# Performance work log

Measured on AMD Instinct MI355X. Metric: run time of the kernel, lower is better.

Reference implementation:

```python
import jax, jax.numpy as jnp
import numpy as np

B_, S_, DIM, DT_RANK, D_STATE = 4, 1024, 384, 24, 16


def layer_norm(x, g, b, eps=1e-5):
    mu = jnp.mean(x, axis=-1, keepdims=True)
    var = jnp.mean((x - mu) ** 2, axis=-1, keepdims=True)
    return (x - mu) * jax.lax.rsqrt(var + eps) * g + b


def conv1d(x, w, b):
    # x: (B, C, L), w: (O, I, K), 'same' padding for odd K
    pad = (w.shape[-1] - 1) // 2
    y = jax.lax.conv_general_dilated(x, w, (1,), [(pad, pad)],
                                     dimension_numbers=('NCH', 'OIH', 'NCH'))
    return y + b[None, :, None]


def ssm(x, w_dbc, w_dt, b_dt, A_log, D):
    # x: (b, s, d) -> selective scan (Mamba), parallel (associative) scan form
    dbc = jnp.einsum('bsd,ed->bse', x, w_dbc)
    delta, Bm, Cm = jnp.split(dbc, [DT_RANK, DT_RANK + D_STATE], axis=-1)
    delta = jax.nn.softplus(jnp.einsum('bsr,dr->bsd', delta, w_dt) + b_dt)  # (b,s,d)
    A = -jnp.exp(A_log)                                   # (d, n)
    deltaA = jnp.exp(delta[..., None] * A)                # (b,s,d,n)
    BX = (delta * x)[..., None] * Bm[:, :, None, :]       # (b,s,d,n)

    def combine(c1, c2):
        a1, h1 = c1
        a2, h2 = c2
        return a1 * a2, a2 * h1 + h2

    _, hs = jax.lax.associative_scan(combine, (deltaA, BX), axis=1)
    y = jnp.einsum('bsdn,bsn->bsd', hs, Cm)
    return y + D * x


def setup_inputs() -> dict:
    key = jax.random.key(0)
    ks = jax.random.split(key, 16)
    sc = 0.02
    d, r, n = DIM, DT_RANK, D_STATE
    A_log = jnp.log(jnp.tile(jnp.arange(1, n + 1, dtype=jnp.float32), (d, 1)))  # (d, n)
    return {
        'x': jax.random.normal(ks[0], (B_, S_, d), dtype=jnp.float32),
        'w_p1': jax.random.normal(ks[1], (d, d, 3)) * sc, 'b_p1': jnp.zeros((d,)),
        'w_p2': jax.random.normal(ks[2], (d, d, 3)) * sc, 'b_p2': jnp.zeros((d,)),
        'w_p3': jax.random.normal(ks[3], (d, d, 1)) * sc, 'b_p3': jnp.zeros((d,)),
        'w_cf': jax.random.normal(ks[4], (d, d, 1)) * sc, 'b_cf': jnp.zeros((d,)),
        'w_cb': jax.random.normal(ks[5], (d, d, 1)) * sc, 'b_cb': jnp.zeros((d,)),
        'g_n': jnp.ones((d,)), 'bt_n': jnp.zeros((d,)),
        'g_nf': jnp.ones((d,)), 'bt_nf': jnp.zeros((d,)),
        'g_nb': jnp.ones((d,)), 'bt_nb': jnp.zeros((d,)),
        'w_dbc1': jax.random.normal(ks[6], (r + 2 * n, d)) * sc,
        'w_dt1': jax.random.normal(ks[7], (d, r)) * sc, 'b_dt1': jnp.zeros((d,)),
        'A_log1': A_log, 'D1': jnp.ones((d,)),
        'w_dbc2': jax.random.normal(ks[8], (r + 2 * n, d)) * sc,
        'w_dt2': jax.random.normal(ks[9], (d, r)) * sc, 'b_dt2': jnp.zeros((d,)),
        'A_log2': A_log, 'D2': jnp.ones((d,)),
    }


def reference(x, w_p1, b_p1, w_p2, b_p2, w_p3, b_p3, w_cf, b_cf, w_cb, b_cb,
              g_n, bt_n, g_nf, bt_nf, g_nb, bt_nb,
              w_dbc1, w_dt1, b_dt1, A_log1, D1,
              w_dbc2, w_dt2, b_dt2, A_log2, D2):
    skip = x
    xn = layer_norm(x, g_n, bt_n)
    xt = jnp.swapaxes(xn, 1, 2)                       # (b, d, s)
    z1 = jnp.swapaxes(conv1d(xt, w_p1, b_p1), 1, 2)   # (b, s, d)
    xp = conv1d(xt, w_p2, b_p2)                       # (b, d, s)

    def direction(xd, wc, bc, g, bt, w_dbc, w_dt, b_dt, A_log, D):
        h = conv1d(xd, wc, bc)
        h = jnp.swapaxes(h, 1, 2)
        h = layer_norm(h, g, bt)
        return ssm(h, w_dbc, w_dt, b_dt, A_log, D)

    x1 = direction(xp, w_cf, b_cf, g_nf, bt_nf, w_dbc1, w_dt1, b_dt1, A_log1, D1)
    # backward direction: sequence flipped (note: original does NOT flip back)
    x2 = direction(xp[:, :, ::-1], w_cb, b_cb, g_nb, bt_nb, w_dbc2, w_dt2, b_dt2, A_log2, D2)

    z = jax.nn.silu(z1)
    x3 = jnp.swapaxes((x1 + x2) * z, 1, 2)            # (b, d, s)
    out = jnp.swapaxes(conv1d(x3, w_p3, b_p3), 1, 2)
    return out + skip
```

## Files before the change

kernel.cpp:

```cpp
#include <hip/hip_runtime.h>
#include <cstddef>

#define NB 4
#define NS 1024
#define ND 384
#define NN 16
#define MTOT 4096
#define TM 8
#define NCH 32
#define CHL 32

static __device__ __forceinline__ float fget(const float4& v, int e) {
    return e == 0 ? v.x : e == 1 ? v.y : e == 2 ? v.z : v.w;
}

__global__ __launch_bounds__(256) void prep_weights(
    const float* __restrict__ w_p1, const float* __restrict__ w_p2,
    const float* __restrict__ w_p3, const float* __restrict__ w_cf,
    const float* __restrict__ w_cb,
    const float* __restrict__ w_dbc1, const float* __restrict__ w_dbc2,
    const float* __restrict__ w_dt1,  const float* __restrict__ w_dt2,
    float* __restrict__ wp1P, float* __restrict__ wp2P, float* __restrict__ wp3P,
    float* __restrict__ wcfP, float* __restrict__ wcbP,
    float* __restrict__ wdbc1P, float* __restrict__ wdbc2P,
    float* __restrict__ wdt1T,  float* __restrict__ wdt2T)
{
    int idx = blockIdx.x * 256 + threadIdx.x;
    if (idx < 884736) {
        int q = idx; const float* w; float* wT;
        if (q < 442368) { w = w_p1; wT = wp1P; }
        else            { q -= 442368; w = w_p2; wT = wp2P; }
        int e = q & 3; int o = (q >> 2) % 384; int kk = q / 1536;
        int k = kk / 96; int i = (kk % 96) * 4 + e;
        wT[q] = w[((size_t)o * 384 + i) * 3 + k];
    } else if (idx < 1327104) {
        int q = idx - 884736; const float* w; float* wT;
        if (q < 147456)      { w = w_p3; wT = wp3P; }
        else if (q < 294912) { q -= 147456; w = w_cf; wT = wcfP; }
        else                 { q -= 294912; w = w_cb; wT = wcbP; }
        int e = q & 3; int o = (q >> 2) % 384; int i = (q / 1536) * 4 + e;
        wT[q] = w[(size_t)o * 384 + i];
    } else if (idx < 1370112) {
        int q = idx - 1327104; const float* w; float* wT;
        if (q < 21504) { w = w_dbc1; wT = wdbc1P; }
        else           { q -= 21504; w = w_dbc2; wT = wdbc2P; }
        int e = q & 3; int oc = (q >> 2) % 56; int i = (q / 224) * 4 + e;
        wT[q] = w[(size_t)oc * 384 + i];
    } else if (idx < 1388544) {
        int q = idx - 1370112; const float* w; float* wT;
        if (q < 9216) { w = w_dt1; wT = wdt1T; }
        else          { q -= 9216; w = w_dt2; wT = wdt2T; }
        int d = q % 384; int qq = q / 384;
        wT[q] = w[(size_t)d * 24 + qq];
    }
}

__global__ __launch_bounds__(384) void conv3x2(
    const float* __restrict__ x,
    const float* __restrict__ g_n, const float* __restrict__ bt_n,
    const float* __restrict__ wp2P, const float* __restrict__ b_p2,
    const float* __restrict__ wp1P, const float* __restrict__ b_p1,
    float* __restrict__ XP, float* __restrict__ Z1)
{
    __shared__ float xn[TM + 2][ND];
    int m0 = blockIdx.x * TM;
    int b = m0 >> 10, s0 = m0 & 1023;
    int t = threadIdx.x, wid = t >> 6, lane = t & 63;

    for (int j = wid; j < TM + 2; j += 6) {
        int r = s0 - 1 + j;
        if (r < 0 || r >= NS) {
            for (int e = 0; e < 6; ++e) xn[j][lane + 64 * e] = 0.f;
        } else {
            const float* row = x + ((size_t)(b * NS + r)) * ND;
            float v[6]; float s1 = 0.f, s2 = 0.f;
            #pragma unroll
            for (int e = 0; e < 6; ++e) {
                v[e] = row[lane + 64 * e];
                s1 += v[e]; s2 += v[e] * v[e];
            }
            #pragma unroll
            for (int o = 32; o; o >>= 1) {
                s1 += __shfl_xor(s1, o);
                s2 += __shfl_xor(s2, o);
            }
            float mu = s1 * (1.f / ND);
            float var = s2 * (1.f / ND) - mu * mu;
            float rs = rsqrtf(var + 1e-5f);
            #pragma unroll
            for (int e = 0; e < 6; ++e) {
                int i = lane + 64 * e;
                xn[j][i] = (v[e] - mu) * rs * g_n[i] + bt_n[i];
            }
        }
    }
    __syncthreads();

    const float4* xnf4 = reinterpret_cast<const float4*>(&xn[0][0]);
    const float4* w2f4 = reinterpret_cast<const float4*>(wp2P) + t;
    const float4* w1f4 = reinterpret_cast<const float4*>(wp1P) + t;

    float a2[TM], a1[TM];
    #pragma unroll
    for (int r = 0; r < TM; ++r) { a2[r] = b_p2[t]; a1[r] = b_p1[t]; }

    float4 W2c = w2f4[0], W1c = w1f4[0];
    for (int kk = 0; kk < 288; ++kk) {
        int kn = (kk < 287) ? kk + 1 : 287;
        float4 W2n = w2f4[(size_t)kn * 384];
        float4 W1n = w1f4[(size_t)kn * 384];
        float4 xv[TM];
        #pragma unroll
        for (int r = 0; r < TM; ++r) xv[r] = xnf4[r * 96 + kk];
        #pragma unroll
        for (int e = 0; e < 4; ++e) {
            float wv2 = fget(W2c, e);
            float wv1 = fget(W1c, e);
            #pragma unroll
            for (int r = 0; r < TM; ++r) {
                float xe = fget(xv[r], e);
                a2[r] = fmaf(xe, wv2, a2[r]);
                a1[r] = fmaf(xe, wv1, a1[r]);
            }
        }
        W2c = W2n; W1c = W1n;
    }
    #pragma unroll
    for (int r = 0; r < TM; ++r) {
        size_t ix = (size_t)(m0 + r) * ND + t;
        XP[ix] = a2[r];
        Z1[ix] = a1[r];
    }
}

__global__ __launch_bounds__(384) void dir2_k1(
    const float* __restrict__ XP,
    const float* __restrict__ wcfP, const float* __restrict__ b_cf,
    const float* __restrict__ g_nf, const float* __restrict__ bt_nf,
    const float* __restrict__ wdbc1P, const float* __restrict__ wdt1T,
    const float* __restrict__ b_dt1,
    const float* __restrict__ wcbP, const float* __restrict__ b_cb,
    const float* __restrict__ g_nb, const float* __restrict__ bt_nb,
    const float* __restrict__ wdbc2P, const float* __restrict__ wdt2T,
    const float* __restrict__ b_dt2,
    float* __restrict__ LN2, float* __restrict__ DBC2, float* __restrict__ DEL2)
{
    __shared__ float xp[TM][ND];
    __shared__ float uo[TM][ND];
    __shared__ float red[TM][6][2];
    __shared__ float dbcS[TM][56];
    int blk = blockIdx.x;
    int dir = blk >> 9;
    int m0 = (blk & 511) * TM;
    int b = m0 >> 10, s0 = m0 & 1023;
    int t = threadIdx.x, wid = t >> 6, lane = t & 63;

    const float* wcP   = dir ? wcbP   : wcfP;
    const float* b_c   = dir ? b_cb   : b_cf;
    const float* g     = dir ? g_nb   : g_nf;
    const float* bt    = dir ? bt_nb  : bt_nf;
    const float* wdbcP = dir ? wdbc2P : wdbc1P;
    const float* wdtT  = dir ? wdt2T  : wdt1T;
    const float* b_dt  = dir ? b_dt2  : b_dt1;
    const size_t NM = (size_t)MTOT * ND;
    float* LNo  = LN2  + (size_t)dir * NM;
    float* DBCo = DBC2 + (size_t)dir * MTOT * 56;
    float* DELo = DEL2 + (size_t)dir * NM;

    {
        float4* xpf4 = reinterpret_cast<float4*>(&xp[0][0]);
        const float4* XPf4 = reinterpret_cast<const float4*>(XP);
        for (int e = t; e < TM * 96; e += 384) {
            int j = e / 96, i4 = e - (e / 96) * 96;
            int s = s0 + j;
            int sE = dir ? (NS - 1 - s) : s;
            xpf4[j * 96 + i4] = XPf4[((size_t)(b * NS + sE)) * 96 + i4];
        }
    }
    __syncthreads();

    const float4* xpf4 = reinterpret_cast<const float4*>(&xp[0][0]);
    const float4* wcf4 = reinterpret_cast<const float4*>(wcP) + t;
    float acc[TM];
    #pragma unroll
    for (int r = 0; r < TM; ++r) acc[r] = b_c[t];
    float4 Wc = wcf4[0];
    for (int i4 = 0; i4 < 96; ++i4) {
        int in_ = (i4 < 95) ? i4 + 1 : 95;
        float4 Wn = wcf4[(size_t)in_ * 384];
        float4 xv[TM];
        #pragma unroll
        for (int r = 0; r < TM; ++r) xv[r] = xpf4[r * 96 + i4];
        #pragma unroll
        for (int e = 0; e < 4; ++e) {
            float wv = fget(Wc, e);
            #pragma unroll
            for (int r = 0; r < TM; ++r)
                acc[r] = fmaf(fget(xv[r], e), wv, acc[r]);
        }
        Wc = Wn;
    }

    #pragma unroll
    for (int r = 0; r < TM; ++r) {
        float s1 = acc[r], s2 = acc[r] * acc[r];
        #pragma unroll
        for (int o = 32; o; o >>= 1) {
            s1 += __shfl_xor(s1, o);
            s2 += __shfl_xor(s2, o);
        }
        if (lane == 0) { red[r][wid][0] = s1; red[r][wid][1] = s2; }
    }
    __syncthreads();
    float gt = g[t], btt = bt[t];
    #pragma unroll
    for (int r = 0; r < TM; ++r) {
        float s1 = 0.f, s2 = 0.f;
        #pragma unroll
        for (int w = 0; w < 6; ++w) { s1 += red[r][w][0]; s2 += red[r][w][1]; }
        float mu = s1 * (1.f / ND);
        float var = s2 * (1.f / ND) - mu * mu;
        float rs = rsqrtf(var + 1e-5f);
        float ln = (acc[r] - mu) * rs * gt + btt;
        uo[r][t] = ln;
        LNo[(size_t)(m0 + r) * ND + t] = ln;
    }
    __syncthreads();

    for (int r = wid; r < TM; r += 6) {
        if (lane < 56) {
            const float4* wdf4 = reinterpret_cast<const float4*>(wdbcP) + lane;
            const float4* uof4 = reinterpret_cast<const float4*>(&uo[r][0]);
            float a = 0.f;
            float4 Wd = wdf4[0];
            for (int i4 = 0; i4 < 96; ++i4) {
                int in_ = (i4 < 95) ? i4 + 1 : 95;
                float4 Wdn = wdf4[(size_t)in_ * 56];
                float4 uv = uof4[i4];
                a = fmaf(uv.x, Wd.x, a);
                a = fmaf(uv.y, Wd.y, a);
                a = fmaf(uv.z, Wd.z, a);
                a = fmaf(uv.w, Wd.w, a);
                Wd = Wdn;
            }
            dbcS[r][lane] = a;
            DBCo[(size_t)(m0 + r) * 56 + lane] = a;
        }
    }
    __syncthreads();

    float accD[TM]; float bd = b_dt[t];
    #pragma unroll
    for (int r = 0; r < TM; ++r) accD[r] = bd;
    for (int q = 0; q < 24; ++q) {
        float wv = wdtT[q * 384 + t];
        #pragma unroll
        for (int r = 0; r < TM; ++r) accD[r] = fmaf(dbcS[r][q], wv, accD[r]);
    }
    #pragma unroll
    for (int r = 0; r < TM; ++r) {
        float a = accD[r];
        DELo[(size_t)(m0 + r) * ND + t] =
            fmaxf(a, 0.f) + log1pf(__expf(-fabsf(a)));
    }
}

__global__ __launch_bounds__(384) void scan_s1(
    const float* __restrict__ DEL2, const float* __restrict__ LN2,
    const float* __restrict__ DBC2, const float* __restrict__ A_log1,
    const float* __restrict__ A_log2,
    float* __restrict__ P, float* __restrict__ H)
{
    __shared__ float bc[CHL][32];
    int blk = blockIdx.x;
    int c = blk & (NCH - 1);
    int db = blk >> 5;
    int dir = db >> 2, b = db & 3;
    int t = threadIdx.x;
    const float* del  = DEL2 + (size_t)dir * MTOT * ND;
    const float* u    = LN2  + (size_t)dir * MTOT * ND;
    const float* dbc  = DBC2 + (size_t)dir * MTOT * 56;
    const float* Alog = dir ? A_log2 : A_log1;

    for (int e = t; e < CHL * 32; e += 384) {
        int row = e >> 5, col = e & 31;
        bc[row][col] = dbc[((size_t)(b * NS + c * CHL + row)) * 56 + 24 + col];
    }
    __syncthreads();

    float A[NN], h[NN], p[NN];
    #pragma unroll
    for (int n = 0; n < NN; ++n) {
        A[n] = -__expf(Alog[(size_t)t * NN + n]);
        h[n] = 0.f; p[n] = 1.f;
    }
    for (int j = 0; j < CHL; ++j) {
        size_t rix = (size_t)b * NS + c * CHL + j;
        float dl = del[rix * ND + t];
        float uv = u[rix * ND + t];
        float dx = dl * uv;
        #pragma unroll
        for (int n = 0; n < NN; ++n) {
            float da = __expf(dl * A[n]);
            h[n] = fmaf(da, h[n], dx * bc[j][n]);
            p[n] *= da;
        }
    }
    size_t base = ((size_t)blk * ND + t) * NN;
    #pragma unroll
    for (int n = 0; n < NN; ++n) { P[base + n] = p[n]; H[base + n] = h[n]; }
}

__global__ __launch_bounds__(256) void scan_s2(
    float* __restrict__ P, const float* __restrict__ H)
{
    int gid = blockIdx.x * 256 + threadIdx.x;
    int n = gid & 15;
    int d = (gid >> 4) % ND;
    int db = gid / (16 * ND);
    float h = 0.f;
    for (int c = 0; c < NCH; ++c) {
        size_t idx = (((size_t)db * NCH + c) * ND + d) * NN + n;
        float p = P[idx];
        float hh = H[idx];
        P[idx] = h;
        h = fmaf(p, h, hh);
    }
}

__global__ __launch_bounds__(384) void scan_s3(
    const float* __restrict__ DEL2, const float* __restrict__ LN2,
    const float* __restrict__ DBC2, const float* __restrict__ A_log1,
    const float* __restrict__ A_log2, const float* __restrict__ D1,
    const float* __restrict__ D2, const float* __restrict__ Hinit,
    float* __restrict__ Y2)
{
    __shared__ float bc[CHL][32];
    int blk = blockIdx.x;
    int c = blk & (NCH - 1);
    int db = blk >> 5;
    int dir = db >> 2, b = db & 3;
    int t = threadIdx.x;
    const float* del  = DEL2 + (size_t)dir * MTOT * ND;
    const float* u    = LN2  + (size_t)dir * MTOT * ND;
    const float* dbc  = DBC2 + (size_t)dir * MTOT * 56;
    const float* Alog = dir ? A_log2 : A_log1;
    const float* Dv   = dir ? D2 : D1;
    float* y          = Y2 + (size_t)dir * MTOT * ND;

    for (int e = t; e < CHL * 32; e += 384) {
        int row = e >> 5, col = e & 31;
        bc[row][col] = dbc[((size_t)(b * NS + c * CHL + row)) * 56 + 24 + col];
    }
    __syncthreads();

    size_t base = ((size_t)blk * ND + t) * NN;
    float A[NN], h[NN];
    #pragma unroll
    for (int n = 0; n < NN; ++n) {
        A[n] = -__expf(Alog[(size_t)t * NN + n]);
        h[n] = Hinit[base + n];
    }
    float Dd = Dv[t];
    for (int j = 0; j < CHL; ++j) {
        size_t rix = (size_t)b * NS + c * CHL + j;
        float dl = del[rix * ND + t];
        float uv = u[rix * ND + t];
        float dx = dl * uv;
        float y0 = 0.f, y1 = 0.f;
        #pragma unroll
        for (int n = 0; n < NN; n += 2) {
            float da0 = __expf(dl * A[n]);
            float da1 = __expf(dl * A[n + 1]);
            h[n]     = fmaf(da0, h[n],     dx * bc[j][n]);
            h[n + 1] = fmaf(da1, h[n + 1], dx * bc[j][n + 1]);
            y0 = fmaf(h[n],     bc[j][16 + n],     y0);
            y1 = fmaf(h[n + 1], bc[j][16 + n + 1], y1);
        }
        y[rix * ND + t] = y0 + y1 + Dd * uv;
    }
}

__global__ __launch_bounds__(64) void scan2(
    const float* __restrict__ DEL2, const float* __restrict__ LN2,
    const float* __restrict__ DBC2, const float* __restrict__ A1,
    const float* __restrict__ D1v, const float* __restrict__ A2,
    const float* __restrict__ D2v, float* __restrict__ Y2)
{
    int gid = blockIdx.x * 64 + threadIdx.x;
    int dir = gid >= (NB * ND);
    int gd = gid - dir * (NB * ND);
    const float* delta = DEL2 + (size_t)dir * MTOT * ND;
    const float* u     = LN2  + (size_t)dir * MTOT * ND;
    const float* dbc   = DBC2 + (size_t)dir * MTOT * 56;
    const float* Alog  = dir ? A2 : A1;
    const float* Dv    = dir ? D2v : D1v;
    float* y_out       = Y2 + (size_t)dir * MTOT * ND;

    int d = gd % ND, b = gd / ND;
    float A[NN], h[NN];
    #pragma unroll
    for (int n = 0; n < NN; ++n) {
        A[n] = -__expf(Alog[(size_t)d * NN + n]);
        h[n] = 0.f;
    }
    float Dd = Dv[d];
    for (int s = 0; s < NS; ++s) {
        size_t rix = (size_t)b * NS + s;
        float dl = delta[rix * ND + d];
        float uv = u[rix * ND + d];
        float dx = dl * uv;
        const float* r = dbc + rix * 56;
        float y0 = 0.f, y1 = 0.f;
        #pragma unroll
        for (int n = 0; n < NN; n += 2) {
            float da0 = __expf(dl * A[n]);
            float da1 = __expf(dl * A[n + 1]);
            h[n]     = fmaf(da0, h[n],     dx * r[24 + n]);
            h[n + 1] = fmaf(da1, h[n + 1], dx * r[24 + n + 1]);
            y0 = fmaf(h[n],     r[40 + n],     y0);
            y1 = fmaf(h[n + 1], r[40 + n + 1], y1);
        }
        y_out[rix * ND + d] = y0 + y1 + Dd * uv;
    }
}

__global__ __launch_bounds__(384) void final_k(
    const float* __restrict__ x, const float* __restrict__ Z1,
    const float* __restrict__ YF, const float* __restrict__ YB,
    const float* __restrict__ wp3P, const float* __restrict__ b_p3,
    float* __restrict__ out)
{
    __shared__ float x3[TM][ND];
    int m0 = blockIdx.x * TM;
    int t = threadIdx.x;
    #pragma unroll
    for (int r = 0; r < TM; ++r) {
        size_t ix = (size_t)(m0 + r) * ND + t;
        float z = Z1[ix];
        float sz = z / (1.f + __expf(-z));
        x3[r][t] = (YF[ix] + YB[ix]) * sz;
    }
    __syncthreads();

    const float4* x3f4 = reinterpret_cast<const float4*>(&x3[0][0]);
    const float4* wpf4 = reinterpret_cast<const float4*>(wp3P) + t;
    float acc[TM]; float bp = b_p3[t];
    #pragma unroll
    for (int r = 0; r < TM; ++r) acc[r] = bp;
    float4 Wp = wpf4[0];
    for (int i4 = 0; i4 < 96; ++i4) {
        int in_ = (i4 < 95) ? i4 + 1 : 95;
        float4 Wn = wpf4[(size_t)in_ * 384];
        float4 xv[TM];
        #pragma unroll
        for (int r = 0; r < TM; ++r) xv[r] = x3f4[r * 96 + i4];
        #pragma unroll
        for (int e = 0; e < 4; ++e) {
            float wv = fget(Wp, e);
            #pragma unroll
            for (int r = 0; r < TM; ++r)
                acc[r] = fmaf(fget(xv[r], e), wv, acc[r]);
        }
        Wp = Wn;
    }
    #pragma unroll
    for (int r = 0; r < TM; ++r) {
        size_t ix = (size_t)(m0 + r) * ND + t;
        out[ix] = acc[r] + x[ix];
    }
}

__global__ __launch_bounds__(256) void fill_f32(float* out, float v, int n)
{
    int i = blockIdx.x * 256 + threadIdx.x;
    if (i < n) out[i] = v;
}

extern "C" void kernel_launch(void* const* d_in, const int* in_sizes, int n_in,
                              void* d_out, int out_size, void* d_ws, size_t ws_size,
                              hipStream_t stream) {
    float* out = (float*)d_out;

    if (out_size != MTOT * ND) {
        fill_f32<<<(out_size + 255) / 256, 256, 0, stream>>>(
            out, 70000.f + (float)(out_size >> 16), out_size);
        return;
    }

    const float* x      = (const float*)d_in[0];
    const float* w_p1   = (const float*)d_in[1];
    const float* b_p1   = (const float*)d_in[2];
    const float* w_p2   = (const float*)d_in[3];
    const float* b_p2   = (const float*)d_in[4];
    const float* w_p3   = (const float*)d_in[5];
    const float* b_p3   = (const float*)d_in[6];
    const float* w_cf   = (const float*)d_in[7];
    const float* b_cf   = (const float*)d_in[8];
    const float* w_cb   = (const float*)d_in[9];
    const float* b_cb   = (const float*)d_in[10];
    const float* g_n    = (const float*)d_in[11];
    const float* bt_n   = (const float*)d_in[12];
    const float* g_nf   = (const float*)d_in[13];
    const float* bt_nf  = (const float*)d_in[14];
    const float* g_nb   = (const float*)d_in[15];
    const float* bt_nb  = (const float*)d_in[16];
    const float* w_dbc1 = (const float*)d_in[17];
    const float* w_dt1  = (const float*)d_in[18];
    const float* b_dt1  = (const float*)d_in[19];
    const float* A_log1 = (const float*)d_in[20];
    const float* D1     = (const float*)d_in[21];
    const float* w_dbc2 = (const float*)d_in[22];
    const float* w_dt2  = (const float*)d_in[23];
    const float* b_dt2  = (const float*)d_in[24];
    const float* A_log2 = (const float*)d_in[25];
    const float* D2     = (const float*)d_in[26];

    const size_t NM = (size_t)MTOT * ND;
    const size_t N56 = (size_t)MTOT * 56;
    const size_t AGG = (size_t)2 * NB * NCH * ND * NN;
    size_t off = 0;
    float* ws = (float*)d_ws;
    float* XP    = ws + off; off += NM;
    float* Z1    = ws + off; off += NM;
    float* LN2   = ws + off; off += 2 * NM;
    float* DEL2  = ws + off; off += 2 * NM;
    float* Y2    = ws + off; off += 2 * NM;
    float* DBC2  = ws + off; off += 2 * N56;
    float* wp1P   = ws + off; off += 442368;
    float* wp2P   = ws + off; off += 442368;
    float* wp3P   = ws + off; off += 147456;
    float* wcfP   = ws + off; off += 147456;
    float* wcbP   = ws + off; off += 147456;
    float* wdbc1P = ws + off; off += 21504;
    float* wdbc2P = ws + off; off += 21504;
    float* wdt1T  = ws + off; off += 9216;
    float* wdt2T  = ws + off; off += 9216;
    const size_t ws_base = off;
    float* Pagg  = ws + off; off += AGG;
    float* Hagg  = ws + off; off += AGG;
    const size_t ws_fast = off;

    if (ws_size < ws_base * sizeof(float)) {
        fill_f32<<<(out_size + 255) / 256, 256, 0, stream>>>(out, 60000.f, out_size);
        return;
    }
    const int fast_scan = (ws_size >= ws_fast * sizeof(float));

    float* YF   = Y2;         float* YB   = Y2 + NM;

    prep_weights<<<5424, 256, 0, stream>>>(
        w_p1, w_p2, w_p3, w_cf, w_cb, w_dbc1, w_dbc2, w_dt1, w_dt2,
        wp1P, wp2P, wp3P, wcfP, wcbP, wdbc1P, wdbc2P, wdt1T, wdt2T);

    conv3x2<<<MTOT / TM, 384, 0, stream>>>(
        x, g_n, bt_n, wp2P, b_p2, wp1P, b_p1, XP, Z1);

    dir2_k1<<<2 * (MTOT / TM), 384, 0, stream>>>(
        XP,
        wcfP, b_cf, g_nf, bt_nf, wdbc1P, wdt1T, b_dt1,
        wcbP, b_cb, g_nb, bt_nb, wdbc2P, wdt2T, b_dt2,
        LN2, DBC2, DEL2);

    if (fast_scan) {
        scan_s1<<<2 * NB * NCH, 384, 0, stream>>>(
            DEL2, LN2, DBC2, A_log1, A_log2, Pagg, Hagg);
        scan_s2<<<(2 * NB * ND * NN) / 256, 256, 0, stream>>>(Pagg, Hagg);
        scan_s3<<<2 * NB * NCH, 384, 0, stream>>>(
            DEL2, LN2, DBC2, A_log1, A_log2, D1, D2, Pagg, Y2);
    } else {
        scan2<<<(2 * NB * ND) / 64, 64, 0, stream>>>(
            DEL2, LN2, DBC2, A_log1, D1, A_log2, D2, Y2);
    }

    final_k<<<MTOT / TM, 384, 0, stream>>>(
        x, Z1, YF, YB, wp3P, b_p3, out);
}
```

Before: 426.0 us.

## Split layernorm and gating into separate kernels, read GEMM operands from global

After: 433.9 us. About the same (+1.9%).

```diff
diff --git a/kernel.cpp b/kernel.cpp
--- a/kernel.cpp
+++ b/kernel.cpp
@@ -9,6 +9,7 @@
 #define TM 8
 #define NCH 32
 #define CHL 32
+#define NSP (NS + 2)
 
 static __device__ __forceinline__ float fget(const float4& v, int e) {
     return e == 0 ? v.x : e == 1 ? v.y : e == 2 ? v.z : v.w;
@@ -55,48 +56,58 @@
     }
 }
 
-__global__ __launch_bounds__(384) void conv3x2(
+__global__ __launch_bounds__(384) void ln1_k(
     const float* __restrict__ x,
     const float* __restrict__ g_n, const float* __restrict__ bt_n,
+    float* __restrict__ XNP)
+{
+    int blk = blockIdx.x;
+    int t = threadIdx.x, wid = t >> 6, lane = t & 63;
+    if (blk == MTOT / TM) {
+        for (int b = 0; b < NB; ++b) {
+            XNP[((size_t)b * NSP + 0) * ND + t] = 0.f;
+            XNP[((size_t)b * NSP + NS + 1) * ND + t] = 0.f;
+        }
+        return;
+    }
+    int m0 = blk * TM;
+    int b = m0 >> 10, s0 = m0 & 1023;
+    for (int j = wid; j < TM; j += 6) {
+        int r = s0 + j;
+        const float* row = x + ((size_t)(b * NS + r)) * ND;
+        float v[6]; float s1 = 0.f, s2 = 0.f;
+        #pragma unroll
+        for (int e = 0; e < 6; ++e) {
+            v[e] = row[lane + 64 * e];
+            s1 += v[e]; s2 += v[e] * v[e];
+        }
+        #pragma unroll
+        for (int o = 32; o; o >>= 1) {
+            s1 += __shfl_xor(s1, o);
+            s2 += __shfl_xor(s2, o);
+        }
+        float mu = s1 * (1.f / ND);
+        float var = s2 * (1.f / ND) - mu * mu;
+        float rs = rsqrtf(var + 1e-5f);
+        float* orow = XNP + ((size_t)b * NSP + r + 1) * ND;
+        #pragma unroll
+        for (int e = 0; e < 6; ++e) {
+            int i = lane + 64 * e;
+            orow[i] = (v[e] - mu) * rs * g_n[i] + bt_n[i];
+        }
+    }
+}
+
+__global__ __launch_bounds__(384) void conv3x2(
+    const float* __restrict__ XNP,
     const float* __restrict__ wp2P, const float* __restrict__ b_p2,
     const float* __restrict__ wp1P, const float* __restrict__ b_p1,
     float* __restrict__ XP, float* __restrict__ Z1)
 {
-    __shared__ float xn[TM + 2][ND];
     int m0 = blockIdx.x * TM;
     int b = m0 >> 10, s0 = m0 & 1023;
-    int t = threadIdx.x, wid = t >> 6, lane = t & 63;
-
-    for (int j = wid; j < TM + 2; j += 6) {
-        int r = s0 - 1 + j;
-        if (r < 0 || r >= NS) {
-            for (int e = 0; e < 6; ++e) xn[j][lane + 64 * e] = 0.f;
-        } else {
-            const float* row = x + ((size_t)(b * NS + r)) * ND;
-            float v[6]; float s1 = 0.f, s2 = 0.f;
-            #pragma unroll
-            for (int e = 0; e < 6; ++e) {
-                v[e] = row[lane + 64 * e];
-                s1 += v[e]; s2 += v[e] * v[e];
-            }
-            #pragma unroll
-            for (int o = 32; o; o >>= 1) {
-                s1 += __shfl_xor(s1, o);
-                s2 += __shfl_xor(s2, o);
-            }
-            float mu = s1 * (1.f / ND);
-            float var = s2 * (1.f / ND) - mu * mu;
-            float rs = rsqrtf(var + 1e-5f);
-            #pragma unroll
-            for (int e = 0; e < 6; ++e) {
-                int i = lane + 64 * e;
-                xn[j][i] = (v[e] - mu) * rs * g_n[i] + bt_n[i];
-            }
-        }
-    }
-    __syncthreads();
-
-    const float4* xnf4 = reinterpret_cast<const float4*>(&xn[0][0]);
+    int t = threadIdx.x;
+    const float4* xnp4 = reinterpret_cast<const float4*>(XNP);
     const float4* w2f4 = reinterpret_cast<const float4*>(wp2P) + t;
     const float4* w1f4 = reinterpret_cast<const float4*>(wp1P) + t;
 
@@ -105,25 +116,29 @@
     for (int r = 0; r < TM; ++r) { a2[r] = b_p2[t]; a1[r] = b_p1[t]; }
 
     float4 W2c = w2f4[0], W1c = w1f4[0];
-    for (int kk = 0; kk < 288; ++kk) {
-        int kn = (kk < 287) ? kk + 1 : 287;
-        float4 W2n = w2f4[(size_t)kn * 384];
-        float4 W1n = w1f4[(size_t)kn * 384];
-        float4 xv[TM];
-        #pragma unroll
-        for (int r = 0; r < TM; ++r) xv[r] = xnf4[r * 96 + kk];
-        #pragma unroll
-        for (int e = 0; e < 4; ++e) {
-            float wv2 = fget(W2c, e);
-            float wv1 = fget(W1c, e);
+    for (int k = 0; k < 3; ++k) {
+        size_t rb = ((size_t)(b * NSP + s0 + k)) * 96;
+        for (int i4 = 0; i4 < 96; ++i4) {
+            int kk = k * 96 + i4;
+            int kn = (kk < 287) ? kk + 1 : 287;
+            float4 W2n = w2f4[(size_t)kn * 384];
+            float4 W1n = w1f4[(size_t)kn * 384];
+            float4 xv[TM];
             #pragma unroll
-            for (int r = 0; r < TM; ++r) {
-                float xe = fget(xv[r], e);
-                a2[r] = fmaf(xe, wv2, a2[r]);
-                a1[r] = fmaf(xe, wv1, a1[r]);
+            for (int r = 0; r < TM; ++r) xv[r] = xnp4[rb + (size_t)r * 96 + i4];
+            #pragma unroll
+            for (int e = 0; e < 4; ++e) {
+                float wv2 = fget(W2c, e);
+                float wv1 = fget(W1c, e);
+                #pragma unroll
+                for (int r = 0; r < TM; ++r) {
+                    float xe = fget(xv[r], e);
+                    a2[r] = fmaf(xe, wv2, a2[r]);
+                    a1[r] = fmaf(xe, wv1, a1[r]);
+                }
             }
-        }
-        W2c = W2n; W1c = W1n;
+            W2c = W2n; W1c = W1n;
+        }
     }
     #pragma unroll
     for (int r = 0; r < TM; ++r) {
@@ -145,7 +160,6 @@
     const float* __restrict__ b_dt2,
     float* __restrict__ LN2, float* __restrict__ DBC2, float* __restrict__ DEL2)
 {
-    __shared__ float xp[TM][ND];
     __shared__ float uo[TM][ND];
     __shared__ float red[TM][6][2];
     __shared__ float dbcS[TM][56];
@@ -167,19 +181,15 @@
     float* DBCo = DBC2 + (size_t)dir * MTOT * 56;
     float* DELo = DEL2 + (size_t)dir * NM;
 
-    {
-        float4* xpf4 = reinterpret_cast<float4*>(&xp[0][0]);
-        const float4* XPf4 = reinterpret_cast<const float4*>(XP);
-        for (int e = t; e < TM * 96; e += 384) {
-            int j = e / 96, i4 = e - (e / 96) * 96;
-            int s = s0 + j;
-            int sE = dir ? (NS - 1 - s) : s;
-            xpf4[j * 96 + i4] = XPf4[((size_t)(b * NS + sE)) * 96 + i4];
-        }
-    }
-    __syncthreads();
-
-    const float4* xpf4 = reinterpret_cast<const float4*>(&xp[0][0]);
+    const float4* XPf4 = reinterpret_cast<const float4*>(XP);
+    size_t rowb[TM];
+    #pragma unroll
+    for (int r = 0; r < TM; ++r) {
+        int s = s0 + r;
+        int sE = dir ? (NS - 1 - s) : s;
+        rowb[r] = ((size_t)(b * NS + sE)) * 96;
+    }
+
     const float4* wcf4 = reinterpret_cast<const float4*>(wcP) + t;
     float acc[TM];
     #pragma unroll
@@ -190,7 +200,7 @@
         float4 Wn = wcf4[(size_t)in_ * 384];
         float4 xv[TM];
         #pragma unroll
-        for (int r = 0; r < TM; ++r) xv[r] = xpf4[r * 96 + i4];
+        for (int r = 0; r < TM; ++r) xv[r] = XPf4[rowb[r] + i4];
         #pragma unroll
         for (int e = 0; e < 4; ++e) {
             float wv = fget(Wc, e);
@@ -425,26 +435,34 @@
     }
 }
 
+__global__ __launch_bounds__(256) void gate_k(
+    const float* __restrict__ Z1, const float* __restrict__ YF,
+    const float* __restrict__ YB, float* __restrict__ X3)
+{
+    int i = blockIdx.x * 256 + threadIdx.x;
+    const float4* z4 = reinterpret_cast<const float4*>(Z1);
+    const float4* f4 = reinterpret_cast<const float4*>(YF);
+    const float4* b4 = reinterpret_cast<const float4*>(YB);
+    float4* o4 = reinterpret_cast<float4*>(X3);
+    float4 z = z4[i], f = f4[i], bb = b4[i], o;
+    o.x = (f.x + bb.x) * (z.x / (1.f + __expf(-z.x)));
+    o.y = (f.y + bb.y) * (z.y / (1.f + __expf(-z.y)));
+    o.z = (f.z + bb.z) * (z.z / (1.f + __expf(-z.z)));
+    o.w = (f.w + bb.w) * (z.w / (1.f + __expf(-z.w)));
+    o4[i] = o;
+}
+
 __global__ __launch_bounds__(384) void final_k(
-    const float* __restrict__ x, const float* __restrict__ Z1,
-    const float* __restrict__ YF, const float* __restrict__ YB,
+    const float* __restrict__ x, const float* __restrict__ X3,
     const float* __restrict__ wp3P, const float* __restrict__ b_p3,
     float* __restrict__ out)
 {
-    __shared__ float x3[TM][ND];
     int m0 = blockIdx.x * TM;
     int t = threadIdx.x;
-    #pragma unroll
-    for (int r = 0; r < TM; ++r) {
-        size_t ix = (size_t)(m0 + r) * ND + t;
-        float z = Z1[ix];
-        float sz = z / (1.f + __expf(-z));
-        x3[r][t] = (YF[ix] + YB[ix]) * sz;
-    }
-    __syncthreads();
-
-    const float4* x3f4 = reinterpret_cast<const float4*>(&x3[0][0]);
+    const float4* x3f4 = reinterpret_cast<const float4*>(X3);
     const float4* wpf4 = reinterpret_cast<const float4*>(wp3P) + t;
+    size_t rb = (size_t)m0 * 96;
+
     float acc[TM]; float bp = b_p3[t];
     #pragma unroll
     for (int r = 0; r < TM; ++r) acc[r] = bp;
@@ -454,7 +472,7 @@
         float4 Wn = wpf4[(size_t)in_ * 384];
         float4 xv[TM];
         #pragma unroll
-        for (int r = 0; r < TM; ++r) xv[r] = x3f4[r * 96 + i4];
+        for (int r = 0; r < TM; ++r) xv[r] = x3f4[rb + (size_t)r * 96 + i4];
         #pragma unroll
         for (int e = 0; e < 4; ++e) {
             float wv = fget(Wp, e);
@@ -548,13 +566,17 @@
     const int fast_scan = (ws_size >= ws_fast * sizeof(float));
 
     float* YF   = Y2;         float* YB   = Y2 + NM;
+    float* XNP = Y2;
+    float* X3  = DEL2;
 
     prep_weights<<<5424, 256, 0, stream>>>(
         w_p1, w_p2, w_p3, w_cf, w_cb, w_dbc1, w_dbc2, w_dt1, w_dt2,
         wp1P, wp2P, wp3P, wcfP, wcbP, wdbc1P, wdbc2P, wdt1T, wdt2T);
 
+    ln1_k<<<MTOT / TM + 1, 384, 0, stream>>>(x, g_n, bt_n, XNP);
+
     conv3x2<<<MTOT / TM, 384, 0, stream>>>(
-        x, g_n, bt_n, wp2P, b_p2, wp1P, b_p1, XP, Z1);
+        XNP, wp2P, b_p2, wp1P, b_p1, XP, Z1);
 
     dir2_k1<<<2 * (MTOT / TM), 384, 0, stream>>>(
         XP,
@@ -573,6 +595,8 @@
             DEL2, LN2, DBC2, A_log1, D1, A_log2, D2, Y2);
     }
 
+    gate_k<<<(int)(NM / 4 / 256), 256, 0, stream>>>(Z1, YF, YB, X3);
+
     final_k<<<MTOT / TM, 384, 0, stream>>>(
-        x, Z1, YF, YB, wp3P, b_p3, out);
-}
+        x, X3, wp3P, b_p3, out);
+}
```
